# Kernel optimization log

Hardware: AMD Instinct MI355X
Metric: run time of the kernel (lower is better)

Reference implementation:

```python
import jax, jax.numpy as jnp
import numpy as np

B, H, W, C = 32, 32, 32, 512
N_GROUPS = 32
EPS = 1e-5


def group_norm(x, scale, bias, n_groups=N_GROUPS, eps=EPS):
    b, h, w, c = x.shape
    xg = x.reshape(b, h, w, n_groups, c // n_groups)
    mean = xg.mean(axis=(1, 2, 4), keepdims=True)
    var = xg.var(axis=(1, 2, 4), keepdims=True)
    xg = (xg - mean) * jax.lax.rsqrt(var + eps)
    return xg.reshape(b, h, w, c) * scale + bias


def setup_inputs() -> dict:
    key = jax.random.key(0)
    ks = jax.random.split(key, 8)
    x = jax.random.normal(ks[0], (B, H, W, C), dtype=jnp.float32)
    t = jax.random.normal(ks[1], (B,), dtype=jnp.float32)
    gn_scale = jnp.ones((C,), jnp.float32)
    gn_bias = jnp.zeros((C,), jnp.float32)
    w_qkv = jax.random.normal(ks[2], (C, 3 * C), dtype=jnp.float32) / np.sqrt(C)
    b_qkv = jnp.zeros((3 * C,), jnp.float32)
    w_out = jax.random.normal(ks[3], (C, C), dtype=jnp.float32) / np.sqrt(C)
    b_out = jnp.zeros((C,), jnp.float32)
    return {"x": x, "t": t, "gn_scale": gn_scale, "gn_bias": gn_bias,
            "w_qkv": w_qkv, "b_qkv": b_qkv, "w_out": w_out, "b_out": b_out}


def reference(x, t, gn_scale, gn_bias, w_qkv, b_qkv, w_out, b_out):
    b, h, w, c = x.shape
    z = group_norm(x, gn_scale, gn_bias)
    qkv = jnp.einsum('bhwc,cd->bhwd', z, w_qkv) + b_qkv  # [b,h,w,3C]
    q, k, v = jnp.split(qkv, 3, axis=-1)
    # single-head spatial attention over all h*w positions
    attn = jnp.einsum('bhwc,bHWc->bhwHW', q, k) / jnp.sqrt(jnp.asarray(c, x.dtype))
    attn = jax.nn.softmax(attn.reshape(b, h, w, h * w), axis=-1)
    attn = attn.reshape(b, h, w, h, w)
    scores = jnp.einsum('bhwHW,bHWc->bhwc', attn, v)
    scores = jnp.einsum('bhwc,cd->bhwd', scores, w_out) + b_out
    return x + scores
```

## Files before the change

kernel.cpp:

```cpp
#include <hip/hip_runtime.h>

typedef unsigned short u16;
typedef short bf16x8 __attribute__((ext_vector_type(8)));
typedef float f32x4 __attribute__((ext_vector_type(4)));

__device__ __forceinline__ u16 f2bf(float f) {
  union { float f; unsigned u; } c; c.f = f;
  unsigned r = (c.u + 0x7FFFu + ((c.u >> 16) & 1u)) >> 16;
  return (u16)r;
}
__device__ __forceinline__ float bf2f(u16 h) {
  union { unsigned u; float f; } c; c.u = ((unsigned)h) << 16;
  return c.f;
}
__device__ __forceinline__ void gload16(const void* g, void* l) {
  __builtin_amdgcn_global_load_lds(
      (const __attribute__((address_space(1))) unsigned*)g,
      (__attribute__((address_space(3))) unsigned*)l, 16, 0, 0);
}

__global__ __launch_bounds__(256) void prep_weights(
    const float* __restrict__ w_qkv, const float* __restrict__ w_out,
    u16* __restrict__ wqkvT, u16* __restrict__ woutT) {
  int i = blockIdx.x * 256 + threadIdx.x;
  const int T1 = 1536 * 512;
  if (i < T1) {
    int n = i >> 9, c = i & 511;
    wqkvT[i] = f2bf(w_qkv[(size_t)c * 1536 + n]);
  } else {
    int j = i - T1;
    int n = j >> 9, c = j & 511;
    woutT[j] = f2bf(w_out[(size_t)c * 512 + n]);
  }
}

__global__ __launch_bounds__(256) void groupnorm_k(
    const float* __restrict__ x, const float* __restrict__ scale,
    const float* __restrict__ bias, u16* __restrict__ z) {
  const int blk = blockIdx.x, b = blk >> 5, g = blk & 31;
  const float* xb = x + (size_t)b * 524288 + g * 16;
  u16* zb = z + (size_t)b * 524288 + g * 16;
  const int tid = threadIdx.x, lane = tid & 63, wid = tid >> 6;

  float4 vv[16];
  float s = 0.f, ss = 0.f;
#pragma unroll
  for (int i = 0; i < 16; ++i) {
    int e = (i * 256 + tid) * 4;
    int hw = e >> 4, j = e & 15;
    vv[i] = *(const float4*)&xb[(size_t)hw * 512 + j];
    s += vv[i].x + vv[i].y + vv[i].z + vv[i].w;
    ss += vv[i].x * vv[i].x + vv[i].y * vv[i].y + vv[i].z * vv[i].z + vv[i].w * vv[i].w;
  }
#pragma unroll
  for (int off = 32; off; off >>= 1) {
    s += __shfl_xor(s, off);
    ss += __shfl_xor(ss, off);
  }
  __shared__ float rs[4], rq[4];
  if (!lane) { rs[wid] = s; rq[wid] = ss; }
  __syncthreads();
  float S_ = rs[0] + rs[1] + rs[2] + rs[3];
  float Q_ = rq[0] + rq[1] + rq[2] + rq[3];
  const float inv_n = 1.f / 16384.f;
  float mean = S_ * inv_n;
  float var = Q_ * inv_n - mean * mean;
  float rstd = rsqrtf(var + 1e-5f);

  int j0 = (tid * 4) & 15;
  float sc0 = scale[g * 16 + j0 + 0] * rstd, sc1 = scale[g * 16 + j0 + 1] * rstd;
  float sc2 = scale[g * 16 + j0 + 2] * rstd, sc3 = scale[g * 16 + j0 + 3] * rstd;
  float bi0 = bias[g * 16 + j0 + 0] - mean * sc0, bi1 = bias[g * 16 + j0 + 1] - mean * sc1;
  float bi2 = bias[g * 16 + j0 + 2] - mean * sc2, bi3 = bias[g * 16 + j0 + 3] - mean * sc3;
#pragma unroll
  for (int i = 0; i < 16; ++i) {
    int e = (i * 256 + tid) * 4;
    int hw = e >> 4, j = e & 15;
    ushort4 o;
    o.x = f2bf(vv[i].x * sc0 + bi0);
    o.y = f2bf(vv[i].y * sc1 + bi1);
    o.z = f2bf(vv[i].z * sc2 + bi2);
    o.w = f2bf(vv[i].w * sc3 + bi3);
    *(ushort4*)&zb[(size_t)hw * 512 + j] = o;
  }
}

#define QSCALE 0.04419417382415922f

template <int EPI>
__global__ __launch_bounds__(512, 2) void gemm8p(
    const u16* __restrict__ A, const u16* __restrict__ Bt,
    int gx, int gxy, int N, int K,
    int sched, int sp1, int sp2,
    long long sAb, long long sBb, long long sCb,
    const float* __restrict__ bias, const float* __restrict__ resid,
    u16* __restrict__ qb, u16* __restrict__ kb, u16* __restrict__ vt,
    u16* __restrict__ outb, float* __restrict__ outf,
    float* __restrict__ lsum) {
  const int orig = blockIdx.x;
  const int xcd = orig & 7, jj = orig >> 3;
  int id;
  if (sched == 0) {
    int pan = jj % gx, loc = jj / gx;
    id = (xcd * sp1 + loc) * gx + pan;
  } else {
    int tile = jj % gxy, bl = jj / gxy;
    id = (xcd * sp2 + bl) * gxy + tile;
  }
  const int z = id / gxy;
  const int r2 = id - z * gxy;
  const int by = r2 / gx, bx = r2 - by * gx;

  const u16* Ab = A + (size_t)z * sAb;
  const u16* Bb = Bt + (size_t)z * sBb;

  __shared__ u16 As[2][2][8192];
  __shared__ u16 Bs[2][2][8192];

  const int tid = threadIdx.x;
  const int lane = tid & 63, wid = tid >> 6;
  const int wm = wid & 1, wn = wid >> 1;
  const int l15 = lane & 15, l4 = lane >> 4;
  const int m0 = by * 256, n0 = bx * 256;

  const int own_is_b = wid >> 2;
  const int own_h = (wid >> 1) & 1;
  const int prow = ((wid & 1) << 6) | lane;
  const int srow = prow >> 3;
  const int scol = ((prow & 7) ^ (srow & 7)) << 3;
  const u16* own_base = (own_is_b ? Bb : Ab) +
      (size_t)((own_is_b ? n0 : m0) + own_h * 128 + srow) * K + scol;
  const int ldsbase = ((wid & 1) << 6) * 8;

  f32x4 acc[8][4];
#pragma unroll
  for (int i = 0; i < 8; ++i)
#pragma unroll
    for (int j = 0; j < 4; ++j)
#pragma unroll
      for (int r = 0; r < 4; ++r) acc[i][j][r] = 0.f;

  const int NT = K >> 6;

  auto stage = [&](int k0, int buf) {
    u16* l0 = (own_is_b ? &Bs[buf][own_h][0] : &As[buf][own_h][0]) + ldsbase;
    const u16* g0 = own_base + k0;
#pragma unroll
    for (int j = 0; j < 8; ++j)
      gload16(g0 + (size_t)(j * 16) * K, l0 + j * 1024);
  };

  stage(0, 0);
  asm volatile("s_waitcnt vmcnt(0)" ::: "memory");
  __builtin_amdgcn_s_barrier();

  for (int t = 0; t < NT; ++t) {
    const int cur = t & 1;
    const bool pre = (t + 1 < NT);
    const u16* Ah = &As[cur][wm][0];
    const u16* Bh = &Bs[cur][wn >> 1][0];
    const int rbB = (wn & 1) << 6;
    bf16x8 bq[4][2];
#pragma unroll
    for (int q = 0; q < 4; ++q) {
      bf16x8 af[2][2];
      if (q == 0) {
#pragma unroll
        for (int i = 0; i < 4; ++i) {
          const int rr = rbB + i * 16 + l15;
          const int sw = rr & 7;
          bq[i][0] = *(const bf16x8*)&Bh[rr * 64 + ((l4 ^ sw) << 3)];
          bq[i][1] = *(const bf16x8*)&Bh[rr * 64 + (((4 + l4) ^ sw) << 3)];
        }
      }
#pragma unroll
      for (int j = 0; j < 2; ++j) {
        const int rr = (q * 2 + j) * 16 + l15;
        const int sw = rr & 7;
        af[j][0] = *(const bf16x8*)&Ah[rr * 64 + ((l4 ^ sw) << 3)];
        af[j][1] = *(const bf16x8*)&Ah[rr * 64 + (((4 + l4) ^ sw) << 3)];
      }
      if (q == 0 && pre) stage((t + 1) << 6, cur ^ 1);
      __builtin_amdgcn_s_barrier();
      asm volatile("s_waitcnt lgkmcnt(0)" ::: "memory");
      __builtin_amdgcn_sched_barrier(0);
      __builtin_amdgcn_s_setprio(1);
#pragma unroll
      for (int j = 0; j < 2; ++j)
#pragma unroll
        for (int ni = 0; ni < 4; ++ni) {
          acc[q * 2 + j][ni] = __builtin_amdgcn_mfma_f32_16x16x32_bf16(
              af[j][0], bq[ni][0], acc[q * 2 + j][ni], 0, 0, 0);
          acc[q * 2 + j][ni] = __builtin_amdgcn_mfma_f32_16x16x32_bf16(
              af[j][1], bq[ni][1], acc[q * 2 + j][ni], 0, 0, 0);
        }
      __builtin_amdgcn_s_setprio(0);
      if (q == 3 && pre) asm volatile("s_waitcnt vmcnt(0)" ::: "memory");
      __builtin_amdgcn_s_barrier();
    }
  }

  if (EPI == 0) {
#pragma unroll
    for (int mi = 0; mi < 8; ++mi) {
#pragma unroll
      for (int ni = 0; ni < 4; ++ni) {
        const int gr0 = m0 + wm * 128 + mi * 16 + l4 * 4;
        const int gc = n0 + wn * 64 + ni * 16 + l15;
        const int bsel = gc >> 9, cin = gc & 511;
        const float bs = bias[gc];
        if (bsel < 2) {
          u16* dst = bsel ? kb : qb;
#pragma unroll
          for (int r = 0; r < 4; ++r) {
            float vvv = acc[mi][ni][r] + bs;
            if (bsel == 0) vvv *= QSCALE;
            dst[(size_t)(gr0 + r) * 512 + cin] = f2bf(vvv);
          }
        } else {
          ushort4 o;
          o.x = f2bf(acc[mi][ni][0] + bs);
          o.y = f2bf(acc[mi][ni][1] + bs);
          o.z = f2bf(acc[mi][ni][2] + bs);
          o.w = f2bf(acc[mi][ni][3] + bs);
          const int bb = gr0 >> 10, p = gr0 & 1023;
          *(ushort4*)&vt[(size_t)bb * 524288 + (size_t)cin * 1024 + p] = o;
        }
      }
    }
  } else if (EPI == 2) {
#pragma unroll
    for (int mi = 0; mi < 8; ++mi) {
#pragma unroll
      for (int ni = 0; ni < 4; ++ni) {
        const int gr0 = m0 + wm * 128 + mi * 16 + l4 * 4;
        const int gc = n0 + wn * 64 + ni * 16 + l15;
#pragma unroll
        for (int r = 0; r < 4; ++r)
          outf[(size_t)(gr0 + r) * N + gc] =
              acc[mi][ni][r] + bias[gc] + resid[(size_t)(gr0 + r) * N + gc];
      }
    }
  } else if (EPI == 3) {
    float rs_[8][4];
#pragma unroll
    for (int mi = 0; mi < 8; ++mi)
#pragma unroll
      for (int r = 0; r < 4; ++r) rs_[mi][r] = 0.f;
#pragma unroll
    for (int mi = 0; mi < 8; ++mi) {
      const int gr0 = m0 + wm * 128 + mi * 16 + l4 * 4;
#pragma unroll
      for (int ni = 0; ni < 4; ++ni) {
        const int gc = n0 + wn * 64 + ni * 16 + l15;
#pragma unroll
        for (int r = 0; r < 4; ++r) {
          float e = __expf(acc[mi][ni][r]);
          rs_[mi][r] += e;
          outb[(size_t)z * sCb + (size_t)(gr0 + r) * N + gc] = f2bf(e);
        }
      }
    }
#pragma unroll
    for (int mi = 0; mi < 8; ++mi) {
      const int gr0 = m0 + wm * 128 + mi * 16 + l4 * 4;
#pragma unroll
      for (int r = 0; r < 4; ++r) {
        float v = rs_[mi][r];
        v += __shfl_xor(v, 1);
        v += __shfl_xor(v, 2);
        v += __shfl_xor(v, 4);
        v += __shfl_xor(v, 8);
        if (l15 == 0)
          lsum[((size_t)z * 1024 + gr0 + r) * 16 + bx * 4 + wn] = v;
      }
    }
  } else {
#pragma unroll
    for (int mi = 0; mi < 8; ++mi) {
      const int gr0 = m0 + wm * 128 + mi * 16 + l4 * 4;
      float inv[4];
#pragma unroll
      for (int r = 0; r < 4; ++r) {
        const float* lp = &lsum[((size_t)z * 1024 + gr0 + r) * 16];
        const float4 a0 = *(const float4*)&lp[0];
        const float4 a1 = *(const float4*)&lp[4];
        const float4 a2 = *(const float4*)&lp[8];
        const float4 a3 = *(const float4*)&lp[12];
        inv[r] = 1.0f / (a0.x + a0.y + a0.z + a0.w + a1.x + a1.y + a1.z + a1.w +
                         a2.x + a2.y + a2.z + a2.w + a3.x + a3.y + a3.z + a3.w);
      }
#pragma unroll
      for (int ni = 0; ni < 4; ++ni) {
        const int gc = n0 + wn * 64 + ni * 16 + l15;
#pragma unroll
        for (int r = 0; r < 4; ++r)
          outb[(size_t)z * sCb + (size_t)(gr0 + r) * N + gc] =
              f2bf(acc[mi][ni][r] * inv[r]);
      }
    }
  }
}

extern "C" void kernel_launch(void* const* d_in, const int* in_sizes, int n_in,
                              void* d_out, int out_size, void* d_ws, size_t ws_size,
                              hipStream_t stream) {
  const float* x = (const float*)d_in[0];
  const float* gn_scale = (const float*)d_in[2];
  const float* gn_bias = (const float*)d_in[3];
  const float* w_qkv = (const float*)d_in[4];
  const float* b_qkv = (const float*)d_in[5];
  const float* w_out = (const float*)d_in[6];
  const float* b_out = (const float*)d_in[7];
  float* out = (float*)d_out;

  char* ws = (char*)d_ws;
  const size_t MB = 1024ull * 1024ull;
  u16* qb = (u16*)(ws + 0 * MB);
  u16* kb = (u16*)(ws + 32 * MB);
  u16* vt = (u16*)(ws + 64 * MB);
  float* lsum = (float*)(ws + 96 * MB);
  u16* zO = (u16*)(ws + 128 * MB);
  u16* S = (u16*)(ws + 160 * MB);
  u16* wqkvT = (u16*)(ws + 224 * MB);
  u16* woutT = (u16*)(ws + 226 * MB);

  prep_weights<<<4096, 256, 0, stream>>>(w_qkv, w_out, wqkvT, woutT);
  groupnorm_k<<<1024, 256, 0, stream>>>(x, gn_scale, gn_bias, zO);

  gemm8p<0><<<768, 512, 0, stream>>>(
      zO, wqkvT, 6, 768, 1536, 512, 0, 16, 0, 0, 0, 0, b_qkv, nullptr,
      qb, kb, vt, nullptr, nullptr, nullptr);

  gemm8p<3><<<512, 512, 0, stream>>>(
      qb, kb, 4, 16, 1024, 512, 1, 0, 4, 1024 * 512, 1024 * 512, 1024 * 1024,
      nullptr, nullptr, nullptr, nullptr, nullptr, S, nullptr, lsum);

  gemm8p<4><<<256, 512, 0, stream>>>(
      S, vt, 2, 8, 512, 1024, 1, 0, 4, 1024 * 1024, 512 * 1024, 1024 * 512,
      nullptr, nullptr, nullptr, nullptr, nullptr, zO, nullptr, lsum);

  gemm8p<2><<<256, 512, 0, stream>>>(
      zO, woutT, 2, 256, 512, 512, 0, 16, 0, 0, 0, 0, b_out, x,
      nullptr, nullptr, nullptr, nullptr, out, nullptr);
}
```

Measured before the change: 270.7 us.

## Make GEMM blocks loop over multiple N tiles with cross-tile prefetch

Adds a template parameter T so each GEMM block computes T consecutive 256-wide N tiles in sequence. The k-loop pipeline continues across tile boundaries: the first k-slice of the next tile is prefetched while the current tile finishes. Grids for the QKV and QK^T GEMMs shrink to 256 blocks, aiming to remove partial tail waves and per-block launch/prologue cost. The tradeoff is fewer resident blocks per CU, so less latency hiding, and each tile's epilogue runs serially with no overlap.

```diff
diff --git a/kernel.cpp b/kernel.cpp
--- a/kernel.cpp
+++ b/kernel.cpp
@@ -87,7 +87,7 @@
 
 #define QSCALE 0.04419417382415922f
 
-template <int EPI>
+template <int EPI, int T>
 __global__ __launch_bounds__(512, 2) void gemm8p(
     const u16* __restrict__ A, const u16* __restrict__ Bt,
     int gx, int gxy, int N, int K,
@@ -109,7 +109,7 @@
   }
   const int z = id / gxy;
   const int r2 = id - z * gxy;
-  const int by = r2 / gx, bx = r2 - by * gx;
+  const int by = r2 / gx, bx0 = r2 - by * gx;
 
   const u16* Ab = A + (size_t)z * sAb;
   const u16* Bb = Bt + (size_t)z * sBb;
@@ -121,15 +121,14 @@
   const int lane = tid & 63, wid = tid >> 6;
   const int wm = wid & 1, wn = wid >> 1;
   const int l15 = lane & 15, l4 = lane >> 4;
-  const int m0 = by * 256, n0 = bx * 256;
+  const int m0 = by * 256;
 
   const int own_is_b = wid >> 2;
   const int own_h = (wid >> 1) & 1;
   const int prow = ((wid & 1) << 6) | lane;
   const int srow = prow >> 3;
   const int scol = ((prow & 7) ^ (srow & 7)) << 3;
-  const u16* own_base = (own_is_b ? Bb : Ab) +
-      (size_t)((own_is_b ? n0 : m0) + own_h * 128 + srow) * K + scol;
+  const u16* ownA = Ab + (size_t)(m0 + own_h * 128 + srow) * K + scol;
   const int ldsbase = ((wid & 1) << 6) * 8;
 
   f32x4 acc[8][4];
@@ -141,163 +140,189 @@
       for (int r = 0; r < 4; ++r) acc[i][j][r] = 0.f;
 
   const int NT = K >> 6;
-
-  auto stage = [&](int k0, int buf) {
+  const int NTm = NT - 1;
+  const int ntl = (NT == 8) ? 3 : 4;
+  const int G = NT * T;
+
+  auto stage = [&](int k0, int buf, int n0t) {
     u16* l0 = (own_is_b ? &Bs[buf][own_h][0] : &As[buf][own_h][0]) + ldsbase;
-    const u16* g0 = own_base + k0;
+    const u16* g0 = own_is_b
+        ? Bb + (size_t)(n0t + own_h * 128 + srow) * K + scol + k0
+        : ownA + k0;
 #pragma unroll
     for (int j = 0; j < 8; ++j)
       gload16(g0 + (size_t)(j * 16) * K, l0 + j * 1024);
   };
 
-  stage(0, 0);
+  stage(0, 0, bx0 * T * 256);
   asm volatile("s_waitcnt vmcnt(0)" ::: "memory");
   __builtin_amdgcn_s_barrier();
 
-  for (int t = 0; t < NT; ++t) {
-    const int cur = t & 1;
-    const bool pre = (t + 1 < NT);
-    const u16* Ah = &As[cur][wm][0];
-    const u16* Bh = &Bs[cur][wn >> 1][0];
-    const int rbB = (wn & 1) << 6;
-    bf16x8 bq[4][2];
-#pragma unroll
-    for (int q = 0; q < 4; ++q) {
-      bf16x8 af[2][2];
-      if (q == 0) {
-#pragma unroll
-        for (int i = 0; i < 4; ++i) {
-          const int rr = rbB + i * 16 + l15;
+#pragma unroll 1
+  for (int ts = 0; ts < T; ++ts) {
+    const int n0 = (bx0 * T + ts) * 256;
+#pragma unroll 1
+    for (int t = 0; t < NT; ++t) {
+      const int cur = t & 1;
+      const int g = ts * NT + t;
+      const bool pre = (g + 1 < G);
+      const u16* Ah = &As[cur][wm][0];
+      const u16* Bh = &Bs[cur][wn >> 1][0];
+      const int rbB = (wn & 1) << 6;
+      bf16x8 bq[4][2];
+#pragma unroll
+      for (int q = 0; q < 4; ++q) {
+        bf16x8 af[2][2];
+        if (q == 0) {
+#pragma unroll
+          for (int i = 0; i < 4; ++i) {
+            const int rr = rbB + i * 16 + l15;
+            const int sw = rr & 7;
+            bq[i][0] = *(const bf16x8*)&Bh[rr * 64 + ((l4 ^ sw) << 3)];
+            bq[i][1] = *(const bf16x8*)&Bh[rr * 64 + (((4 + l4) ^ sw) << 3)];
+          }
+        }
+#pragma unroll
+        for (int j = 0; j < 2; ++j) {
+          const int rr = (q * 2 + j) * 16 + l15;
           const int sw = rr & 7;
-          bq[i][0] = *(const bf16x8*)&Bh[rr * 64 + ((l4 ^ sw) << 3)];
-          bq[i][1] = *(const bf16x8*)&Bh[rr * 64 + (((4 + l4) ^ sw) << 3)];
-        }
-      }
-#pragma unroll
-      for (int j = 0; j < 2; ++j) {
-        const int rr = (q * 2 + j) * 16 + l15;
-        const int sw = rr & 7;
-        af[j][0] = *(const bf16x8*)&Ah[rr * 64 + ((l4 ^ sw) << 3)];
-        af[j][1] = *(const bf16x8*)&Ah[rr * 64 + (((4 + l4) ^ sw) << 3)];
-      }
-      if (q == 0 && pre) stage((t + 1) << 6, cur ^ 1);
-      __builtin_amdgcn_s_barrier();
-      asm volatile("s_waitcnt lgkmcnt(0)" ::: "memory");
-      __builtin_amdgcn_sched_barrier(0);
-      __builtin_amdgcn_s_setprio(1);
-#pragma unroll
-      for (int j = 0; j < 2; ++j)
+          af[j][0] = *(const bf16x8*)&Ah[rr * 64 + ((l4 ^ sw) << 3)];
+          af[j][1] = *(const bf16x8*)&Ah[rr * 64 + (((4 + l4) ^ sw) << 3)];
+        }
+        if (q == 0 && pre) {
+          const int gn = g + 1;
+          const int tn = gn & NTm;
+          const int tsn = gn >> ntl;
+          stage(tn << 6, cur ^ 1, (bx0 * T + tsn) * 256);
+        }
+        __builtin_amdgcn_s_barrier();
+        asm volatile("s_waitcnt lgkmcnt(0)" ::: "memory");
+        __builtin_amdgcn_sched_barrier(0);
+        __builtin_amdgcn_s_setprio(1);
+#pragma unroll
+        for (int j = 0; j < 2; ++j)
+#pragma unroll
+          for (int ni = 0; ni < 4; ++ni) {
+            acc[q * 2 + j][ni] = __builtin_amdgcn_mfma_f32_16x16x32_bf16(
+                af[j][0], bq[ni][0], acc[q * 2 + j][ni], 0, 0, 0);
+            acc[q * 2 + j][ni] = __builtin_amdgcn_mfma_f32_16x16x32_bf16(
+                af[j][1], bq[ni][1], acc[q * 2 + j][ni], 0, 0, 0);
+          }
+        __builtin_amdgcn_s_setprio(0);
+        if (q == 3 && pre) asm volatile("s_waitcnt vmcnt(0)" ::: "memory");
+        __builtin_amdgcn_s_barrier();
+      }
+    }
+
+    const int bx = bx0 * T + ts;
+    if (EPI == 0) {
+#pragma unroll
+      for (int mi = 0; mi < 8; ++mi) {
 #pragma unroll
         for (int ni = 0; ni < 4; ++ni) {
-          acc[q * 2 + j][ni] = __builtin_amdgcn_mfma_f32_16x16x32_bf16(
-              af[j][0], bq[ni][0], acc[q * 2 + j][ni], 0, 0, 0);
-          acc[q * 2 + j][ni] = __builtin_amdgcn_mfma_f32_16x16x32_bf16(
-              af[j][1], bq[ni][1], acc[q * 2 + j][ni], 0, 0, 0);
-        }
-      __builtin_amdgcn_s_setprio(0);
-      if (q == 3 && pre) asm volatile("s_waitcnt vmcnt(0)" ::: "memory");
-      __builtin_amdgcn_s_barrier();
+          const int gr0 = m0 + wm * 128 + mi * 16 + l4 * 4;
+          const int gc = n0 + wn * 64 + ni * 16 + l15;
+          const int bsel = gc >> 9, cin = gc & 511;
+          const float bs = bias[gc];
+          if (bsel < 2) {
+            u16* dst = bsel ? kb : qb;
+#pragma unroll
+            for (int r = 0; r < 4; ++r) {
+              float vvv = acc[mi][ni][r] + bs;
+              if (bsel == 0) vvv *= QSCALE;
+              dst[(size_t)(gr0 + r) * 512 + cin] = f2bf(vvv);
+            }
+          } else {
+            ushort4 o;
+            o.x = f2bf(acc[mi][ni][0] + bs);
+            o.y = f2bf(acc[mi][ni][1] + bs);
+            o.z = f2bf(acc[mi][ni][2] + bs);
+            o.w = f2bf(acc[mi][ni][3] + bs);
+            const int bb = gr0 >> 10, p = gr0 & 1023;
+            *(ushort4*)&vt[(size_t)bb * 524288 + (size_t)cin * 1024 + p] = o;
+          }
+        }
+      }
+    } else if (EPI == 2) {
+#pragma unroll
+      for (int mi = 0; mi < 8; ++mi) {
+#pragma unroll
+        for (int ni = 0; ni < 4; ++ni) {
+          const int gr0 = m0 + wm * 128 + mi * 16 + l4 * 4;
+          const int gc = n0 + wn * 64 + ni * 16 + l15;
+#pragma unroll
+          for (int r = 0; r < 4; ++r)
+            outf[(size_t)(gr0 + r) * N + gc] =
+                acc[mi][ni][r] + bias[gc] + resid[(size_t)(gr0 + r) * N + gc];
+        }
+      }
+    } else if (EPI == 3) {
+      float rs_[8][4];
+#pragma unroll
+      for (int mi = 0; mi < 8; ++mi)
+#pragma unroll
+        for (int r = 0; r < 4; ++r) rs_[mi][r] = 0.f;
+#pragma unroll
+      for (int mi = 0; mi < 8; ++mi) {
+        const int gr0 = m0 + wm * 128 + mi * 16 + l4 * 4;
+#pragma unroll
+        for (int ni = 0; ni < 4; ++ni) {
+          const int gc = n0 + wn * 64 + ni * 16 + l15;
+#pragma unroll
+          for (int r = 0; r < 4; ++r) {
+            float e = __expf(acc[mi][ni][r]);
+            rs_[mi][r] += e;
+            outb[(size_t)z * sCb + (size_t)(gr0 + r) * N + gc] = f2bf(e);
+          }
+        }
+      }
+#pragma unroll
+      for (int mi = 0; mi < 8; ++mi) {
+        const int gr0 = m0 + wm * 128 + mi * 16 + l4 * 4;
+#pragma unroll
+        for (int r = 0; r < 4; ++r) {
+          float v = rs_[mi][r];
+          v += __shfl_xor(v, 1);
+          v += __shfl_xor(v, 2);
+          v += __shfl_xor(v, 4);
+          v += __shfl_xor(v, 8);
+          if (l15 == 0)
+            lsum[((size_t)z * 1024 + gr0 + r) * 16 + bx * 4 + wn] = v;
+        }
+      }
+    } else {
+#pragma unroll
+      for (int mi = 0; mi < 8; ++mi) {
+        const int gr0 = m0 + wm * 128 + mi * 16 + l4 * 4;
+        float inv[4];
+#pragma unroll
+        for (int r = 0; r < 4; ++r) {
+          const float* lp = &lsum[((size_t)z * 1024 + gr0 + r) * 16];
+          const float4 a0 = *(const float4*)&lp[0];
+          const float4 a1 = *(const float4*)&lp[4];
+          const float4 a2 = *(const float4*)&lp[8];
+          const float4 a3 = *(const float4*)&lp[12];
+          inv[r] = 1.0f / (a0.x + a0.y + a0.z + a0.w + a1.x + a1.y + a1.z + a1.w +
+                           a2.x + a2.y + a2.z + a2.w + a3.x + a3.y + a3.z + a3.w);
+        }
+#pragma unroll
+        for (int ni = 0; ni < 4; ++ni) {
+          const int gc = n0 + wn * 64 + ni * 16 + l15;
+#pragma unroll
+          for (int r = 0; r < 4; ++r)
+            outb[(size_t)z * sCb + (size_t)(gr0 + r) * N + gc] =
+                f2bf(acc[mi][ni][r] * inv[r]);
+        }
+      }
     }
-  }
-
-  if (EPI == 0) {
-#pragma unroll
-    for (int mi = 0; mi < 8; ++mi) {
-#pragma unroll
-      for (int ni = 0; ni < 4; ++ni) {
-        const int gr0 = m0 + wm * 128 + mi * 16 + l4 * 4;
-        const int gc = n0 + wn * 64 + ni * 16 + l15;
-        const int bsel = gc >> 9, cin = gc & 511;
-        const float bs = bias[gc];
-        if (bsel < 2) {
-          u16* dst = bsel ? kb : qb;
-#pragma unroll
-          for (int r = 0; r < 4; ++r) {
-            float vvv = acc[mi][ni][r] + bs;
-            if (bsel == 0) vvv *= QSCALE;
-            dst[(size_t)(gr0 + r) * 512 + cin] = f2bf(vvv);
-          }
-        } else {
-          ushort4 o;
-          o.x = f2bf(acc[mi][ni][0] + bs);
-          o.y = f2bf(acc[mi][ni][1] + bs);
-          o.z = f2bf(acc[mi][ni][2] + bs);
-          o.w = f2bf(acc[mi][ni][3] + bs);
-          const int bb = gr0 >> 10, p = gr0 & 1023;
-          *(ushort4*)&vt[(size_t)bb * 524288 + (size_t)cin * 1024 + p] = o;
-        }
-      }
-    }
-  } else if (EPI == 2) {
-#pragma unroll
-    for (int mi = 0; mi < 8; ++mi) {
-#pragma unroll
-      for (int ni = 0; ni < 4; ++ni) {
-        const int gr0 = m0 + wm * 128 + mi * 16 + l4 * 4;
-        const int gc = n0 + wn * 64 + ni * 16 + l15;
-#pragma unroll
-        for (int r = 0; r < 4; ++r)
-          outf[(size_t)(gr0 + r) * N + gc] =
-              acc[mi][ni][r] + bias[gc] + resid[(size_t)(gr0 + r) * N + gc];
-      }
-    }
-  } else if (EPI == 3) {
-    float rs_[8][4];
-#pragma unroll
-    for (int mi = 0; mi < 8; ++mi)
-#pragma unroll
-      for (int r = 0; r < 4; ++r) rs_[mi][r] = 0.f;
-#pragma unroll
-    for (int mi = 0; mi < 8; ++mi) {
-      const int gr0 = m0 + wm * 128 + mi * 16 + l4 * 4;
-#pragma unroll
-      for (int ni = 0; ni < 4; ++ni) {
-        const int gc = n0 + wn * 64 + ni * 16 + l15;
-#pragma unroll
-        for (int r = 0; r < 4; ++r) {
-          float e = __expf(acc[mi][ni][r]);
-          rs_[mi][r] += e;
-          outb[(size_t)z * sCb + (size_t)(gr0 + r) * N + gc] = f2bf(e);
-        }
-      }
-    }
-#pragma unroll
-    for (int mi = 0; mi < 8; ++mi) {
-      const int gr0 = m0 + wm * 128 + mi * 16 + l4 * 4;
-#pragma unroll
-      for (int r = 0; r < 4; ++r) {
-        float v = rs_[mi][r];
-        v += __shfl_xor(v, 1);
-        v += __shfl_xor(v, 2);
-        v += __shfl_xor(v, 4);
-        v += __shfl_xor(v, 8);
-        if (l15 == 0)
-          lsum[((size_t)z * 1024 + gr0 + r) * 16 + bx * 4 + wn] = v;
-      }
-    }
-  } else {
-#pragma unroll
-    for (int mi = 0; mi < 8; ++mi) {
-      const int gr0 = m0 + wm * 128 + mi * 16 + l4 * 4;
-      float inv[4];
-#pragma unroll
-      for (int r = 0; r < 4; ++r) {
-        const float* lp = &lsum[((size_t)z * 1024 + gr0 + r) * 16];
-        const float4 a0 = *(const float4*)&lp[0];
-        const float4 a1 = *(const float4*)&lp[4];
-        const float4 a2 = *(const float4*)&lp[8];
-        const float4 a3 = *(const float4*)&lp[12];
-        inv[r] = 1.0f / (a0.x + a0.y + a0.z + a0.w + a1.x + a1.y + a1.z + a1.w +
-                         a2.x + a2.y + a2.z + a2.w + a3.x + a3.y + a3.z + a3.w);
-      }
-#pragma unroll
-      for (int ni = 0; ni < 4; ++ni) {
-        const int gc = n0 + wn * 64 + ni * 16 + l15;
-#pragma unroll
-        for (int r = 0; r < 4; ++r)
-          outb[(size_t)z * sCb + (size_t)(gr0 + r) * N + gc] =
-              f2bf(acc[mi][ni][r] * inv[r]);
-      }
+
+    if (ts + 1 < T) {
+#pragma unroll
+      for (int i = 0; i < 8; ++i)
+#pragma unroll
+        for (int j = 0; j < 4; ++j)
+#pragma unroll
+          for (int r = 0; r < 4; ++r) acc[i][j][r] = 0.f;
     }
   }
 }
@@ -328,19 +353,19 @@
   prep_weights<<<4096, 256, 0, stream>>>(w_qkv, w_out, wqkvT, woutT);
   groupnorm_k<<<1024, 256, 0, stream>>>(x, gn_scale, gn_bias, zO);
 
-  gemm8p<0><<<768, 512, 0, stream>>>(
-      zO, wqkvT, 6, 768, 1536, 512, 0, 16, 0, 0, 0, 0, b_qkv, nullptr,
+  gemm8p<0, 3><<<256, 512, 0, stream>>>(
+      zO, wqkvT, 2, 256, 1536, 512, 0, 16, 0, 0, 0, 0, b_qkv, nullptr,
       qb, kb, vt, nullptr, nullptr, nullptr);
 
-  gemm8p<3><<<512, 512, 0, stream>>>(
-      qb, kb, 4, 16, 1024, 512, 1, 0, 4, 1024 * 512, 1024 * 512, 1024 * 1024,
+  gemm8p<3, 2><<<256, 512, 0, stream>>>(
+      qb, kb, 2, 8, 1024, 512, 1, 0, 4, 1024 * 512, 1024 * 512, 1024 * 1024,
       nullptr, nullptr, nullptr, nullptr, nullptr, S, nullptr, lsum);
 
-  gemm8p<4><<<256, 512, 0, stream>>>(
+  gemm8p<4, 1><<<256, 512, 0, stream>>>(
       S, vt, 2, 8, 512, 1024, 1, 0, 4, 1024 * 1024, 512 * 1024, 1024 * 512,
       nullptr, nullptr, nullptr, nullptr, nullptr, zO, nullptr, lsum);
 
-  gemm8p<2><<<256, 512, 0, stream>>>(
+  gemm8p<2, 1><<<256, 512, 0, stream>>>(
       zO, woutT, 2, 256, 512, 512, 0, 16, 0, 0, 0, 0, b_out, x,
       nullptr, nullptr, nullptr, nullptr, out, nullptr);
 }
```

Result: slower. 299.7 us (+10.7%).

## Replace double-buffered GEMM mainloop with 4-stage ring of K=32 tiles

Applied to the files above, without the earlier changes.

Reworks the shared GEMM main loop from a double-buffered K=64 scheme, with four barriers per tile, to a 4-slot ring of K=32 tiles that prefetches three tiles ahead. It uses partial vmcnt waits and one barrier per tile. All threads now cooperatively load both A and B with a new XOR swizzle, and fragment reads use precomputed offsets. The goal is deeper overlap of global-to-LDS loads with MFMA work and less synchronisation. The trade-off is more loop iterations, each with less MFMA work, and correctness that depends on the hand-tuned vmcnt counts and the unroll-by-4 tail handling.

```diff
diff --git a/kernel.cpp b/kernel.cpp
--- a/kernel.cpp
+++ b/kernel.cpp
@@ -88,7 +88,7 @@
 #define QSCALE 0.04419417382415922f
 
 template <int EPI>
-__global__ __launch_bounds__(512, 2) void gemm8p(
+__global__ __launch_bounds__(512, 2) void gemm_ring(
     const u16* __restrict__ A, const u16* __restrict__ Bt,
     int gx, int gxy, int N, int K,
     int sched, int sp1, int sp2,
@@ -114,8 +114,8 @@
   const u16* Ab = A + (size_t)z * sAb;
   const u16* Bb = Bt + (size_t)z * sBb;
 
-  __shared__ u16 As[2][2][8192];
-  __shared__ u16 Bs[2][2][8192];
+  __shared__ u16 As[4][8192];
+  __shared__ u16 Bs[4][8192];
 
   const int tid = threadIdx.x;
   const int lane = tid & 63, wid = tid >> 6;
@@ -123,14 +123,16 @@
   const int l15 = lane & 15, l4 = lane >> 4;
   const int m0 = by * 256, n0 = bx * 256;
 
-  const int own_is_b = wid >> 2;
-  const int own_h = (wid >> 1) & 1;
-  const int prow = ((wid & 1) << 6) | lane;
-  const int srow = prow >> 3;
-  const int scol = ((prow & 7) ^ (srow & 7)) << 3;
-  const u16* own_base = (own_is_b ? Bb : Ab) +
-      (size_t)((own_is_b ? n0 : m0) + own_h * 128 + srow) * K + scol;
-  const int ldsbase = ((wid & 1) << 6) * 8;
+  const int lrs = tid >> 3;
+  const int g0 = (tid & 7) ^ (lrs & 7);
+  const int ra = (lrs << 1) | (g0 >> 2);
+  const int ko = (g0 & 3) << 3;
+
+  const int lrb = l15 >> 1;
+  const int gg = ((l15 & 1) << 2) | l4;
+  const int gsw = gg ^ lrb;
+  const int aoff = wm * 4096 + lrb * 64 + gsw * 8;
+  const int boff = (wn >> 1) * 4096 + (wn & 1) * 2048 + lrb * 64 + gsw * 8;
 
   f32x4 acc[8][4];
 #pragma unroll
@@ -140,65 +142,66 @@
 #pragma unroll
       for (int r = 0; r < 4; ++r) acc[i][j][r] = 0.f;
 
-  const int NT = K >> 6;
-
-  auto stage = [&](int k0, int buf) {
-    u16* l0 = (own_is_b ? &Bs[buf][own_h][0] : &As[buf][own_h][0]) + ldsbase;
-    const u16* g0 = own_base + k0;
-#pragma unroll
-    for (int j = 0; j < 8; ++j)
-      gload16(g0 + (size_t)(j * 16) * K, l0 + j * 1024);
+  const int NT = K >> 5;
+
+  auto stA = [&](int sb, int t2) {
+    const u16* s0 = Ab + (size_t)(m0 + ra) * K + t2 * 32 + ko;
+    const u16* s1 = Ab + (size_t)(m0 + 128 + ra) * K + t2 * 32 + ko;
+    gload16(s0, &As[sb][tid * 8]);
+    gload16(s1, &As[sb][4096 + tid * 8]);
   };
-
-  stage(0, 0);
-  asm volatile("s_waitcnt vmcnt(0)" ::: "memory");
+  auto stB = [&](int sb, int t2) {
+    const u16* s0 = Bb + (size_t)(n0 + ra) * K + t2 * 32 + ko;
+    const u16* s1 = Bb + (size_t)(n0 + 128 + ra) * K + t2 * 32 + ko;
+    gload16(s0, &Bs[sb][tid * 8]);
+    gload16(s1, &Bs[sb][4096 + tid * 8]);
+  };
+
+#define TILE_BODY(P, TT, DOSTG, WN)                                            \
+  do {                                                                         \
+    if (DOSTG) { stA(((P) + 3) & 3, (TT) + 3); stB(((P) + 3) & 3, (TT) + 3); } \
+    bf16x8 bq[4], af0[4], af1[4];                                              \
+    _Pragma("unroll") for (int ni = 0; ni < 4; ++ni)                           \
+        bq[ni] = *(const bf16x8*)&Bs[P][boff + ni * 512];                      \
+    _Pragma("unroll") for (int i = 0; i < 4; ++i)                              \
+        af0[i] = *(const bf16x8*)&As[P][aoff + i * 512];                       \
+    _Pragma("unroll") for (int i = 0; i < 4; ++i)                              \
+        af1[i] = *(const bf16x8*)&As[P][aoff + 2048 + i * 512];                \
+    __builtin_amdgcn_s_setprio(1);                                             \
+    _Pragma("unroll") for (int i = 0; i < 4; ++i)                              \
+        _Pragma("unroll") for (int ni = 0; ni < 4; ++ni)                       \
+            acc[i][ni] = __builtin_amdgcn_mfma_f32_16x16x32_bf16(              \
+                af0[i], bq[ni], acc[i][ni], 0, 0, 0);                          \
+    _Pragma("unroll") for (int i = 0; i < 4; ++i)                              \
+        _Pragma("unroll") for (int ni = 0; ni < 4; ++ni)                       \
+            acc[4 + i][ni] = __builtin_amdgcn_mfma_f32_16x16x32_bf16(          \
+                af1[i], bq[ni], acc[4 + i][ni], 0, 0, 0);                      \
+    __builtin_amdgcn_s_setprio(0);                                             \
+    if ((WN) == 8) asm volatile("s_waitcnt vmcnt(8)" ::: "memory");            \
+    else if ((WN) == 4) asm volatile("s_waitcnt vmcnt(4)" ::: "memory");       \
+    else if ((WN) == 0) asm volatile("s_waitcnt vmcnt(0)" ::: "memory");       \
+    if ((WN) >= -1) __builtin_amdgcn_s_barrier();                              \
+  } while (0)
+
+  stA(0, 0); stB(0, 0);
+  stA(1, 1); stB(1, 1);
+  stA(2, 2); stB(2, 2);
+  asm volatile("s_waitcnt vmcnt(8)" ::: "memory");
   __builtin_amdgcn_s_barrier();
 
-  for (int t = 0; t < NT; ++t) {
-    const int cur = t & 1;
-    const bool pre = (t + 1 < NT);
-    const u16* Ah = &As[cur][wm][0];
-    const u16* Bh = &Bs[cur][wn >> 1][0];
-    const int rbB = (wn & 1) << 6;
-    bf16x8 bq[4][2];
-#pragma unroll
-    for (int q = 0; q < 4; ++q) {
-      bf16x8 af[2][2];
-      if (q == 0) {
-#pragma unroll
-        for (int i = 0; i < 4; ++i) {
-          const int rr = rbB + i * 16 + l15;
-          const int sw = rr & 7;
-          bq[i][0] = *(const bf16x8*)&Bh[rr * 64 + ((l4 ^ sw) << 3)];
-          bq[i][1] = *(const bf16x8*)&Bh[rr * 64 + (((4 + l4) ^ sw) << 3)];
-        }
-      }
-#pragma unroll
-      for (int j = 0; j < 2; ++j) {
-        const int rr = (q * 2 + j) * 16 + l15;
-        const int sw = rr & 7;
-        af[j][0] = *(const bf16x8*)&Ah[rr * 64 + ((l4 ^ sw) << 3)];
-        af[j][1] = *(const bf16x8*)&Ah[rr * 64 + (((4 + l4) ^ sw) << 3)];
-      }
-      if (q == 0 && pre) stage((t + 1) << 6, cur ^ 1);
-      __builtin_amdgcn_s_barrier();
-      asm volatile("s_waitcnt lgkmcnt(0)" ::: "memory");
-      __builtin_amdgcn_sched_barrier(0);
-      __builtin_amdgcn_s_setprio(1);
-#pragma unroll
-      for (int j = 0; j < 2; ++j)
-#pragma unroll
-        for (int ni = 0; ni < 4; ++ni) {
-          acc[q * 2 + j][ni] = __builtin_amdgcn_mfma_f32_16x16x32_bf16(
-              af[j][0], bq[ni][0], acc[q * 2 + j][ni], 0, 0, 0);
-          acc[q * 2 + j][ni] = __builtin_amdgcn_mfma_f32_16x16x32_bf16(
-              af[j][1], bq[ni][1], acc[q * 2 + j][ni], 0, 0, 0);
-        }
-      __builtin_amdgcn_s_setprio(0);
-      if (q == 3 && pre) asm volatile("s_waitcnt vmcnt(0)" ::: "memory");
-      __builtin_amdgcn_s_barrier();
-    }
-  }
+  int t = 0;
+  for (; t + 7 < NT; t += 4) {
+    TILE_BODY(0, t, 1, 8);
+    TILE_BODY(1, t + 1, 1, 8);
+    TILE_BODY(2, t + 2, 1, 8);
+    TILE_BODY(3, t + 3, 1, 8);
+  }
+  TILE_BODY(0, t, 1, 8);
+  TILE_BODY(1, t + 1, 0, 4);
+  TILE_BODY(2, t + 2, 0, 0);
+  TILE_BODY(3, t + 3, 0, -2);
+
+#undef TILE_BODY
 
   if (EPI == 0) {
 #pragma unroll
@@ -328,19 +331,19 @@
   prep_weights<<<4096, 256, 0, stream>>>(w_qkv, w_out, wqkvT, woutT);
   groupnorm_k<<<1024, 256, 0, stream>>>(x, gn_scale, gn_bias, zO);
 
-  gemm8p<0><<<768, 512, 0, stream>>>(
+  gemm_ring<0><<<768, 512, 0, stream>>>(
       zO, wqkvT, 6, 768, 1536, 512, 0, 16, 0, 0, 0, 0, b_qkv, nullptr,
       qb, kb, vt, nullptr, nullptr, nullptr);
 
-  gemm8p<3><<<512, 512, 0, stream>>>(
+  gemm_ring<3><<<512, 512, 0, stream>>>(
       qb, kb, 4, 16, 1024, 512, 1, 0, 4, 1024 * 512, 1024 * 512, 1024 * 1024,
       nullptr, nullptr, nullptr, nullptr, nullptr, S, nullptr, lsum);
 
-  gemm8p<4><<<256, 512, 0, stream>>>(
+  gemm_ring<4><<<256, 512, 0, stream>>>(
       S, vt, 2, 8, 512, 1024, 1, 0, 4, 1024 * 1024, 512 * 1024, 1024 * 512,
       nullptr, nullptr, nullptr, nullptr, nullptr, zO, nullptr, lsum);
 
-  gemm8p<2><<<256, 512, 0, stream>>>(
+  gemm_ring<2><<<256, 512, 0, stream>>>(
       zO, woutT, 2, 256, 512, 512, 0, 16, 0, 0, 0, 0, b_out, x,
       nullptr, nullptr, nullptr, nullptr, out, nullptr);
 }
```

After: 271.0 us. No clear change (+0.1%).
